# Kernel optimization log

Hardware: AMD Instinct MI355X
Metric: run time of the kernel (lower is better)

The kernel has to match this reference:

```python
import jax, jax.numpy as jnp
import numpy as np

GAMMA = 0.5

def smooth_step(t, gamma=GAMMA):
    # DSelect-k SmoothStep: 0 below -g/2, 1 above g/2, cubic in between.
    tc = jnp.clip(t, -gamma / 2, gamma / 2)
    return (-2.0 / gamma**3) * tc**3 + (3.0 / (2.0 * gamma)) * tc + 0.5

def setup_inputs() -> dict:
    key = jax.random.key(0)
    k1, k2, k3 = jax.random.split(key, 3)
    B, p, k, m = 65536, 1024, 8, 6
    x = jax.random.normal(k1, (B, p), dtype=jnp.float32)
    G_w = jax.random.normal(k2, (k, p), dtype=jnp.float32) / np.sqrt(p)
    G_b = jnp.zeros((k,), dtype=jnp.float32)
    W_w = jax.random.normal(k3, (k * m, p), dtype=jnp.float32) / np.sqrt(p)
    W_b = jnp.zeros((k * m,), dtype=jnp.float32)
    return {"x": x, "G_w": G_w, "G_b": G_b, "W_w": W_w, "W_b": W_b}

def reference(x, G_w, G_b, W_w, W_b):
    B = x.shape[0]
    k = G_w.shape[0]
    m = W_w.shape[0] // k
    n = 2 ** m  # number of experts encoded by m binary gates
    gates = (x @ W_w.T + W_b).reshape(B, k, m)
    z = smooth_step(gates)  # (B, k, m) in [0, 1]
    # per_example_selector: probability of expert e = prod_j (z_j if bit_j(e) else 1-z_j)
    bits = ((np.arange(n)[:, None] >> np.arange(m)[None, :]) & 1).astype(bool)  # (n, m)
    bits = jnp.asarray(bits)
    sel = jnp.prod(jnp.where(bits[None, None, :, :], z[:, :, None, :], 1.0 - z[:, :, None, :]), axis=-1)  # (B, k, n)
    weights = jax.nn.softmax(x @ G_w.T + G_b, axis=1)  # (B, k)
    mixture = jnp.einsum('bk,bkn->bn', weights, sel)  # bmm((B,1,k),(B,k,n)) -> (B, n)
    return mixture
```

## Files before the change

### kernel.cpp

```cpp
#include <hip/hip_runtime.h>

typedef _Float16 half8 __attribute__((ext_vector_type(8)));
typedef float f32x4 __attribute__((ext_vector_type(4)));
typedef float f4 __attribute__((ext_vector_type(4)));

#define P_DIM 1024
#define BM 64
#define NH 8
#define AF_ROW 132

__global__ __launch_bounds__(256) void prep_weights(
    const float* __restrict__ Gw, const float* __restrict__ Gb,
    const float* __restrict__ Ww, const float* __restrict__ Wb,
    _Float16* __restrict__ Wf2, float* __restrict__ biasC) {
  int i = blockIdx.x * 256 + threadIdx.x;
  int j = i & 7;
  int l = (i >> 3) & 63;
  int t = (i >> 9) & 3;
  int S = i >> 11;
  int row = t * 16 + (l & 15);
  int k   = S * 32 + (l >> 4) * 8 + j;
  float v = 0.0f;
  if (row < 48) v = Ww[row * P_DIM + k];
  else if (row < 56) v = Gw[(row - 48) * P_DIM + k];
  Wf2[i] = (_Float16)v;
  if (i < 64) {
    float bv = 0.0f;
    if (i < 48) bv = Wb[i];
    else if (i < 56) bv = Gb[i - 48];
    biasC[i] = bv;
  }
}

#define LOAD_B(dst, c) do { const char* p_ = bg + (size_t)(c) * 8192; \
    dst[0] = *(const half8*)(p_);          dst[1] = *(const half8*)(p_ + 4096); \
    dst[2] = *(const half8*)(p_ + 1024);   dst[3] = *(const half8*)(p_ + 5120); \
    dst[4] = *(const half8*)(p_ + 2048);   dst[5] = *(const half8*)(p_ + 6144); \
    dst[6] = *(const half8*)(p_ + 3072);   dst[7] = *(const half8*)(p_ + 7168); \
  } while (0)

#define BODY(bX, cc) do { \
    f4 aX[4]; \
    { const char* p_ = Abase + (cc) * 256; \
      aX[0] = *(const f4*)(p_);       aX[1] = *(const f4*)(p_ + 16); \
      aX[2] = *(const f4*)(p_ + 128); aX[3] = *(const f4*)(p_ + 144); } \
    half8 h0_, h1_; \
    h0_[0]=(_Float16)aX[0][0]; h0_[1]=(_Float16)aX[0][1]; h0_[2]=(_Float16)aX[0][2]; h0_[3]=(_Float16)aX[0][3]; \
    h0_[4]=(_Float16)aX[1][0]; h0_[5]=(_Float16)aX[1][1]; h0_[6]=(_Float16)aX[1][2]; h0_[7]=(_Float16)aX[1][3]; \
    h1_[0]=(_Float16)aX[2][0]; h1_[1]=(_Float16)aX[2][1]; h1_[2]=(_Float16)aX[2][2]; h1_[3]=(_Float16)aX[2][3]; \
    h1_[4]=(_Float16)aX[3][0]; h1_[5]=(_Float16)aX[3][1]; h1_[6]=(_Float16)aX[3][2]; h1_[7]=(_Float16)aX[3][3]; \
    acc[0] = __builtin_amdgcn_mfma_f32_16x16x32_f16(h0_, bX[0], acc[0], 0, 0, 0); \
    acc[0] = __builtin_amdgcn_mfma_f32_16x16x32_f16(h1_, bX[1], acc[0], 0, 0, 0); \
    acc[1] = __builtin_amdgcn_mfma_f32_16x16x32_f16(h0_, bX[2], acc[1], 0, 0, 0); \
    acc[1] = __builtin_amdgcn_mfma_f32_16x16x32_f16(h1_, bX[3], acc[1], 0, 0, 0); \
    acc[2] = __builtin_amdgcn_mfma_f32_16x16x32_f16(h0_, bX[4], acc[2], 0, 0, 0); \
    acc[2] = __builtin_amdgcn_mfma_f32_16x16x32_f16(h1_, bX[5], acc[2], 0, 0, 0); \
    acc[3] = __builtin_amdgcn_mfma_f32_16x16x32_f16(h0_, bX[6], acc[3], 0, 0, 0); \
    acc[3] = __builtin_amdgcn_mfma_f32_16x16x32_f16(h1_, bX[7], acc[3], 0, 0, 0); \
  } while (0)

__global__ __launch_bounds__(256, 3) void fused_gate(
    const float* __restrict__ x, const _Float16* __restrict__ Wf2,
    const float* __restrict__ biasC, float* __restrict__ out) {
  __shared__ __align__(16) float Af[BM][AF_ROW];
  __shared__ float S[BM][65];

  const int tid  = threadIdx.x;
  const int lane = tid & 63;
  const int w    = tid >> 6;
  const int row0 = blockIdx.x * BM;
  const int l15  = lane & 15;
  const int q    = lane >> 4;

  const char* xg = (const char*)(x + (size_t)(row0 + w * 16) * P_DIM) + lane * 8;
  const char* bg = (const char*)Wf2 + lane * 16;

  char* Aw = (char*)&Af[w * 16][0] + lane * 8;
  const char* Abase = (const char*)&Af[w * 16 + l15][0] + q * 32;

  f32x4 acc[4];
#pragma unroll
  for (int t = 0; t < 4; ++t) acc[t] = (f32x4){0.f, 0.f, 0.f, 0.f};

  float2 pf[16];
#pragma unroll
  for (int i = 0; i < 16; ++i) pf[i] = *(const float2*)(xg + i * 4096);

  half8 bA[8], bB[8];
  LOAD_B(bA, 0);

  for (int h = 0; h < NH; ++h) {
    if (h) __syncthreads();
#pragma unroll
    for (int i = 0; i < 16; ++i)
      *(float2*)(Aw + i * 528) = pf[i];
    __syncthreads();
    const int c0 = h * 2;
    LOAD_B(bB, c0 + 1);
    if (h + 1 < NH) {
#pragma unroll
      for (int i = 0; i < 16; ++i)
        pf[i] = *(const float2*)(xg + i * 4096 + (h + 1) * 512);
    }
    BODY(bA, 0);
    BODY(bB, 1);
    if (h + 1 < NH)
      LOAD_B(bA, c0 + 2);
  }

  __syncthreads();
#pragma unroll
  for (int t = 0; t < 4; ++t) {
    float bias = biasC[16 * t + l15];
#pragma unroll
    for (int rr = 0; rr < 4; ++rr) {
      S[w * 16 + q * 4 + rr][16 * t + l15] = acc[t][rr] + bias;
    }
  }
  __syncthreads();

  const int r2  = tid >> 2;
  const int sub = tid & 3;

  float lg[8];
#pragma unroll
  for (int k = 0; k < 8; ++k) lg[k] = S[r2][48 + k];
  float mx = lg[0];
#pragma unroll
  for (int k = 1; k < 8; ++k) mx = fmaxf(mx, lg[k]);
  float wk[8];
  float ssum = 0.f;
#pragma unroll
  for (int k = 0; k < 8; ++k) { wk[k] = expf(lg[k] - mx); ssum += wk[k]; }
  const float inv = 1.0f / ssum;

  float mix[16];
#pragma unroll
  for (int i = 0; i < 16; ++i) mix[i] = 0.f;

#pragma unroll
  for (int k = 0; k < 8; ++k) {
    float z[6];
#pragma unroll
    for (int j = 0; j < 6; ++j) {
      float tt = S[r2][k * 6 + j];
      float tc = fminf(fmaxf(tt, -0.25f), 0.25f);
      z[j] = fmaf(tc, fmaf(-16.0f * tc, tc, 3.0f), 0.5f);
    }
    float f4v = (sub & 1) ? z[4] : 1.0f - z[4];
    float f5v = (sub & 2) ? z[5] : 1.0f - z[5];
    float wf = wk[k] * inv * f4v * f5v;
    float t2[2], t4[4], t8[8], t16[16];
    t2[0] = 1.0f - z[0]; t2[1] = z[0];
#pragma unroll
    for (int i = 0; i < 2; ++i) { t4[i] = t2[i] * (1.0f - z[1]); t4[i + 2] = t2[i] * z[1]; }
#pragma unroll
    for (int i = 0; i < 4; ++i) { t8[i] = t4[i] * (1.0f - z[2]); t8[i + 4] = t4[i] * z[2]; }
#pragma unroll
    for (int i = 0; i < 8; ++i) { t16[i] = t8[i] * (1.0f - z[3]); t16[i + 8] = t8[i] * z[3]; }
#pragma unroll
    for (int i = 0; i < 16; ++i) mix[i] = fmaf(wf, t16[i], mix[i]);
  }

  float* op = out + (size_t)(row0 + r2) * 64 + sub * 16;
#pragma unroll
  for (int g = 0; g < 4; ++g) {
    float4 o;
    o.x = mix[4 * g + 0]; o.y = mix[4 * g + 1];
    o.z = mix[4 * g + 2]; o.w = mix[4 * g + 3];
    ((float4*)op)[g] = o;
  }
}

extern "C" void kernel_launch(void* const* d_in, const int* in_sizes, int n_in,
                              void* d_out, int out_size, void* d_ws, size_t ws_size,
                              hipStream_t stream) {
  const float* x  = (const float*)d_in[0];
  const float* Gw = (const float*)d_in[1];
  const float* Gb = (const float*)d_in[2];
  const float* Ww = (const float*)d_in[3];
  const float* Wb = (const float*)d_in[4];
  float* out = (float*)d_out;

  _Float16* Wf2  = (_Float16*)d_ws;
  float*    bias = (float*)((char*)d_ws + 64 * P_DIM * sizeof(_Float16));

  const int B = in_sizes[0] / P_DIM;

  prep_weights<<<dim3(256), dim3(256), 0, stream>>>(Gw, Gb, Ww, Wb, Wf2, bias);
  fused_gate<<<dim3(B / BM), dim3(256), 0, stream>>>(x, Wf2, bias, out);
  (void)n_in; (void)out_size; (void)ws_size;
}
```

Measured before the change: 64.58 us.

## Stage x as fp16 in shared memory and split waves over output columns

x tiles are now converted to fp16 before being written to shared memory rather than after the read, which halves LDS footprint and LDS read traffic. The work split changes so each wave owns one 16-column slice of the weight matrix across all 64 rows instead of 16 rows across all columns. Each wave therefore loads only 2 weight fragments per chunk instead of 8, cutting register pressure and global weight reads. The score buffer S now aliases the smaller fp16 array. This assumes 64x65 floats fit in 64x136 halves (16640 vs 17408 bytes), which holds.

```diff
diff --git a/kernel.cpp b/kernel.cpp
--- a/kernel.cpp
+++ b/kernel.cpp
@@ -1,13 +1,13 @@
 #include <hip/hip_runtime.h>
 
 typedef _Float16 half8 __attribute__((ext_vector_type(8)));
+typedef _Float16 half2v __attribute__((ext_vector_type(2)));
 typedef float f32x4 __attribute__((ext_vector_type(4)));
-typedef float f4 __attribute__((ext_vector_type(4)));
 
 #define P_DIM 1024
 #define BM 64
 #define NH 8
-#define AF_ROW 132
+#define AH_ROW 136
 
 __global__ __launch_bounds__(256) void prep_weights(
     const float* __restrict__ Gw, const float* __restrict__ Gb,
@@ -32,38 +32,24 @@
   }
 }
 
-#define LOAD_B(dst, c) do { const char* p_ = bg + (size_t)(c) * 8192; \
+#define LOAD_B(dst, c) do { const char* p_ = bgw + (size_t)(c) * 8192; \
     dst[0] = *(const half8*)(p_);          dst[1] = *(const half8*)(p_ + 4096); \
-    dst[2] = *(const half8*)(p_ + 1024);   dst[3] = *(const half8*)(p_ + 5120); \
-    dst[4] = *(const half8*)(p_ + 2048);   dst[5] = *(const half8*)(p_ + 6144); \
-    dst[6] = *(const half8*)(p_ + 3072);   dst[7] = *(const half8*)(p_ + 7168); \
   } while (0)
 
 #define BODY(bX, cc) do { \
-    f4 aX[4]; \
-    { const char* p_ = Abase + (cc) * 256; \
-      aX[0] = *(const f4*)(p_);       aX[1] = *(const f4*)(p_ + 16); \
-      aX[2] = *(const f4*)(p_ + 128); aX[3] = *(const f4*)(p_ + 144); } \
-    half8 h0_, h1_; \
-    h0_[0]=(_Float16)aX[0][0]; h0_[1]=(_Float16)aX[0][1]; h0_[2]=(_Float16)aX[0][2]; h0_[3]=(_Float16)aX[0][3]; \
-    h0_[4]=(_Float16)aX[1][0]; h0_[5]=(_Float16)aX[1][1]; h0_[6]=(_Float16)aX[1][2]; h0_[7]=(_Float16)aX[1][3]; \
-    h1_[0]=(_Float16)aX[2][0]; h1_[1]=(_Float16)aX[2][1]; h1_[2]=(_Float16)aX[2][2]; h1_[3]=(_Float16)aX[2][3]; \
-    h1_[4]=(_Float16)aX[3][0]; h1_[5]=(_Float16)aX[3][1]; h1_[6]=(_Float16)aX[3][2]; h1_[7]=(_Float16)aX[3][3]; \
-    acc[0] = __builtin_amdgcn_mfma_f32_16x16x32_f16(h0_, bX[0], acc[0], 0, 0, 0); \
-    acc[0] = __builtin_amdgcn_mfma_f32_16x16x32_f16(h1_, bX[1], acc[0], 0, 0, 0); \
-    acc[1] = __builtin_amdgcn_mfma_f32_16x16x32_f16(h0_, bX[2], acc[1], 0, 0, 0); \
-    acc[1] = __builtin_amdgcn_mfma_f32_16x16x32_f16(h1_, bX[3], acc[1], 0, 0, 0); \
-    acc[2] = __builtin_amdgcn_mfma_f32_16x16x32_f16(h0_, bX[4], acc[2], 0, 0, 0); \
-    acc[2] = __builtin_amdgcn_mfma_f32_16x16x32_f16(h1_, bX[5], acc[2], 0, 0, 0); \
-    acc[3] = __builtin_amdgcn_mfma_f32_16x16x32_f16(h0_, bX[6], acc[3], 0, 0, 0); \
-    acc[3] = __builtin_amdgcn_mfma_f32_16x16x32_f16(h1_, bX[7], acc[3], 0, 0, 0); \
+    _Pragma("unroll") \
+    for (int m_ = 0; m_ < 4; ++m_) { \
+      half8 a0_ = *(const half8*)&Ah[m_ * 16 + l15][(cc) * 64 + q8]; \
+      half8 a1_ = *(const half8*)&Ah[m_ * 16 + l15][(cc) * 64 + 32 + q8]; \
+      acc[m_] = __builtin_amdgcn_mfma_f32_16x16x32_f16(a0_, bX[0], acc[m_], 0, 0, 0); \
+      acc[m_] = __builtin_amdgcn_mfma_f32_16x16x32_f16(a1_, bX[1], acc[m_], 0, 0, 0); \
+    } \
   } while (0)
 
 __global__ __launch_bounds__(256, 3) void fused_gate(
     const float* __restrict__ x, const _Float16* __restrict__ Wf2,
     const float* __restrict__ biasC, float* __restrict__ out) {
-  __shared__ __align__(16) float Af[BM][AF_ROW];
-  __shared__ float S[BM][65];
+  __shared__ __align__(16) _Float16 Ah[BM][AH_ROW];
 
   const int tid  = threadIdx.x;
   const int lane = tid & 63;
@@ -71,12 +57,10 @@
   const int row0 = blockIdx.x * BM;
   const int l15  = lane & 15;
   const int q    = lane >> 4;
+  const int q8   = q * 8;
 
   const char* xg = (const char*)(x + (size_t)(row0 + w * 16) * P_DIM) + lane * 8;
-  const char* bg = (const char*)Wf2 + lane * 16;
-
-  char* Aw = (char*)&Af[w * 16][0] + lane * 8;
-  const char* Abase = (const char*)&Af[w * 16 + l15][0] + q * 32;
+  const char* bgw = (const char*)Wf2 + lane * 16 + (size_t)w * 1024;
 
   f32x4 acc[4];
 #pragma unroll
@@ -86,14 +70,18 @@
 #pragma unroll
   for (int i = 0; i < 16; ++i) pf[i] = *(const float2*)(xg + i * 4096);
 
-  half8 bA[8], bB[8];
+  half8 bA[2], bB[2];
   LOAD_B(bA, 0);
 
   for (int h = 0; h < NH; ++h) {
     if (h) __syncthreads();
 #pragma unroll
-    for (int i = 0; i < 16; ++i)
-      *(float2*)(Aw + i * 528) = pf[i];
+    for (int i = 0; i < 16; ++i) {
+      half2v hv;
+      hv[0] = (_Float16)pf[i].x;
+      hv[1] = (_Float16)pf[i].y;
+      *(half2v*)&Ah[w * 16 + i][2 * lane] = hv;
+    }
     __syncthreads();
     const int c0 = h * 2;
     LOAD_B(bB, c0 + 1);
@@ -109,12 +97,17 @@
   }
 
   __syncthreads();
+  float (*S)[65] = (float (*)[65])&Ah[0][0];
+
+  {
+    const int col = w * 16 + l15;
+    const float bias = biasC[col];
 #pragma unroll
-  for (int t = 0; t < 4; ++t) {
-    float bias = biasC[16 * t + l15];
+    for (int m = 0; m < 4; ++m) {
 #pragma unroll
-    for (int rr = 0; rr < 4; ++rr) {
-      S[w * 16 + q * 4 + rr][16 * t + l15] = acc[t][rr] + bias;
+      for (int rr = 0; rr < 4; ++rr) {
+        S[m * 16 + q * 4 + rr][col] = acc[m][rr] + bias;
+      }
     }
   }
   __syncthreads();
```

Measured after the change: 61.88 us. 1.04x faster.
